# Kernel optimization log

Hardware: AMD Instinct MI355X
Metric: run time of the kernel (lower is better)

Reference implementation:

```python
import jax, jax.numpy as jnp
import numpy as np

N, E, G = 30000, 480000, 64
IN, H, L = 24, 512, 6


def setup_inputs() -> dict:
    key = jax.random.key(0)
    ks = jax.random.split(key, 20)
    s = 0.05
    inp = {
        "x": jax.random.normal(ks[0], (N, IN), dtype=jnp.float32),
        "edge_index": jax.random.randint(ks[1], (2, E), 0, N, dtype=jnp.int64),
        "batch": jnp.sort(jax.random.randint(ks[2], (N,), 0, G, dtype=jnp.int64)),
        # node encoder
        "enc_w": jax.random.normal(ks[3], (IN, H), dtype=jnp.float32) * s,
        "enc_b": jnp.zeros((H,), dtype=jnp.float32),
        # per-layer message MLP (stacked over L layers), weights stored [in, out]
        "mlp_w1": jax.random.normal(ks[4], (L, H, H), dtype=jnp.float32) * s,
        "mlp_b1": jnp.zeros((L, H), dtype=jnp.float32),
        "mlp_w2": jax.random.normal(ks[5], (L, H, H), dtype=jnp.float32) * s,
        "mlp_b2": jnp.zeros((L, H), dtype=jnp.float32),
        # per-layer GRUCell params, [in, 3H] layout (gates order: r, z, n)
        "gru_wih": jax.random.normal(ks[6], (L, H, 3 * H), dtype=jnp.float32) * s,
        "gru_whh": jax.random.normal(ks[7], (L, H, 3 * H), dtype=jnp.float32) * s,
        "gru_bih": jnp.zeros((L, 3 * H), dtype=jnp.float32),
        "gru_bhh": jnp.zeros((L, 3 * H), dtype=jnp.float32),
        # head MLP
        "head_w1": jax.random.normal(ks[8], (H, H // 2), dtype=jnp.float32) * s,
        "head_b1": jnp.zeros((H // 2,), dtype=jnp.float32),
        "head_w2": jax.random.normal(ks[9], (H // 2, 1), dtype=jnp.float32) * s,
        "head_b2": jnp.zeros((1,), dtype=jnp.float32),
    }
    return inp


def _forward(x, edge_index, batch, enc_w, enc_b, mlp_w1, mlp_b1, mlp_w2, mlp_b2,
             gru_wih, gru_whh, gru_bih, gru_bhh, head_w1, head_b1, head_w2, head_b2):
    src, dst = edge_index[0], edge_index[1]
    h = x @ enc_w + enc_b  # [N, H]
    for l in range(L):
        # message MLP depends only on x_j, so compute per-node then gather
        msg = jnp.maximum(h @ mlp_w1[l] + mlp_b1[l], 0.0) @ mlp_w2[l] + mlp_b2[l]  # [N, H]
        # scatter-add over edges + self-loop contribution (add_self_loops)
        m = jax.ops.segment_sum(msg[src], dst, num_segments=N) + msg  # [N, H]
        # GRUCell(input=m, hidden=h); torch gate order: reset, update, new
        gi = m @ gru_wih[l] + gru_bih[l]
        gh = h @ gru_whh[l] + gru_bhh[l]
        r = jax.nn.sigmoid(gi[:, :H] + gh[:, :H])
        z = jax.nn.sigmoid(gi[:, H:2 * H] + gh[:, H:2 * H])
        n = jnp.tanh(gi[:, 2 * H:] + r * gh[:, 2 * H:])
        h = (1.0 - z) * n + z * h
    # global mean pool per graph
    sums = jax.ops.segment_sum(h, batch, num_segments=G)
    cnt = jax.ops.segment_sum(jnp.ones((N,), dtype=h.dtype), batch, num_segments=G)
    pooled = sums / jnp.maximum(cnt, 1.0)[:, None]  # [G, H]
    out = jnp.maximum(pooled @ head_w1 + head_b1, 0.0) @ head_w2 + head_b2
    return out[:, 0]  # [G]


def reference(x, edge_index, batch, enc_w, enc_b, mlp_w1, mlp_b1, mlp_w2, mlp_b2,
              gru_wih, gru_whh, gru_bih, gru_bhh, head_w1, head_b1, head_w2, head_b2):
    return _forward(x, edge_index, batch, enc_w, enc_b, mlp_w1, mlp_b1, mlp_w2, mlp_b2,
                    gru_wih, gru_whh, gru_bih, gru_bhh, head_w1, head_b1, head_w2, head_b2)
```

## Files before the change

### kernel.cpp

```cpp
#include <hip/hip_runtime.h>
#include <hip/hip_bf16.h>
#include <math.h>

#define N_NODES 30000
#define N_EDGES 480000
#define N_GRAPH 64
#define DIN 24
#define HD 512
#define NL 6

typedef __hip_bfloat16 bf16;
using short8 = __attribute__((ext_vector_type(8))) short;
using f32x4 = __attribute__((ext_vector_type(4))) float;

#define ASYNC16(gp, lp)                                              \
    __builtin_amdgcn_global_load_lds(                                \
        (const __attribute__((address_space(1))) void*)(gp),         \
        (__attribute__((address_space(3))) void*)(lp), 16, 0, 0)

#define WAITALL_BAR()                                                \
    do {                                                             \
        asm volatile("s_waitcnt vmcnt(0) lgkmcnt(0)" ::: "memory");  \
        __builtin_amdgcn_sched_barrier(0);                           \
        __builtin_amdgcn_s_barrier();                                \
    } while (0)

__device__ __forceinline__ float sigmoidf_(float x) { return 1.0f / (1.0f + expf(-x)); }
__device__ __forceinline__ float b2f(unsigned short u) {
    return __uint_as_float(((unsigned int)u) << 16);
}
__device__ __forceinline__ unsigned short f2b(float f) {
    bf16 b = __float2bfloat16(f);
    return *(unsigned short*)&b;
}

__global__ __launch_bounds__(256) void enc_kernel(const float* __restrict__ x,
                                                  const float* __restrict__ w,
                                                  const float* __restrict__ b,
                                                  bf16* __restrict__ h) {
    __shared__ float xs[DIN];
    int row = blockIdx.x;
    int tid = threadIdx.x;
    if (tid < DIN) xs[tid] = x[row * DIN + tid];
    __syncthreads();
    for (int c = tid; c < HD; c += 256) {
        float acc = b[c];
#pragma unroll
        for (int k = 0; k < DIN; k++) acc = fmaf(xs[k], w[k * HD + c], acc);
        h[(size_t)row * HD + c] = __float2bfloat16(acc);
    }
}

__global__ __launch_bounds__(256) void twcvt_kernel(const float* __restrict__ W,
                                                    bf16* __restrict__ WtH,
                                                    bf16* __restrict__ WtL, int Nc) {
    __shared__ float s[32][33];
    int l = blockIdx.z;
    const float* Wp = W + (size_t)l * HD * Nc;
    size_t ob = (size_t)l * HD * Nc;
    int k0 = blockIdx.y * 32, c0 = blockIdx.x * 32;
    int tx = threadIdx.x & 31, ty = threadIdx.x >> 5;
    for (int r = ty; r < 32; r += 8) s[r][tx] = Wp[(size_t)(k0 + r) * Nc + c0 + tx];
    __syncthreads();
    for (int r = ty; r < 32; r += 8) {
        float v = s[tx][r];
        unsigned short hu = f2b(v);
        float hf = b2f(hu);
        size_t o = ob + (size_t)(c0 + r) * HD + k0 + tx;
        *(unsigned short*)&WtH[o] = hu;
        WtL[o] = __float2bfloat16(v - hf);
    }
}

template <bool RELU>
__global__ __launch_bounds__(256, 3) void gemm_mfma(const bf16* __restrict__ A,
                                                    const bf16* __restrict__ WtH,
                                                    const bf16* __restrict__ WtL,
                                                    const float* __restrict__ bias,
                                                    bf16* __restrict__ C, int n) {
    __shared__ __align__(16) bf16 SB[2][3 * 128 * 32];
    int tid = threadIdx.x;
    int wv = tid >> 6, lane = tid & 63;
    int quad = lane >> 4, l16 = lane & 15;
    int crow = lane >> 2, cseg = lane & 3;
    int gseg = cseg ^ ((crow >> 1) & 3);
    int fsw = (quad ^ ((l16 >> 1) & 3)) * 8;
    int row0 = blockIdx.y * 128, col0 = blockIdx.x * 128;
    f32x4 acc[2][8] = {};

    const bf16* gsrc[6];
#pragma unroll
    for (int j = 0; j < 6; j++) {
        int c = wv * 6 + j;
        if (c < 8) {
            int gr = row0 + c * 16 + crow;
            if (gr > n - 1) gr = n - 1;
            gsrc[j] = A + (size_t)gr * HD + gseg * 8;
        } else if (c < 16) {
            gsrc[j] = WtH + (size_t)(col0 + (c - 8) * 16 + crow) * HD + gseg * 8;
        } else {
            gsrc[j] = WtL + (size_t)(col0 + (c - 16) * 16 + crow) * HD + gseg * 8;
        }
    }
    auto stage = [&](int kt, int nb) {
#pragma unroll
        for (int j = 0; j < 6; j++) ASYNC16(gsrc[j] + kt, &SB[nb][(wv * 6 + j) * 512]);
    };

    stage(0, 0);
    for (int t16 = 0; t16 < 16; t16++) {
        int b = t16 & 1;
        WAITALL_BAR();
        if (t16 < 15) stage((t16 + 1) * 32, b ^ 1);
        short8 bfr[2][2];
#pragma unroll
        for (int t = 0; t < 2; t++) {
            int fo = ((wv * 2 + t) * 16 + l16) * 32 + fsw;
            bfr[t][0] = *(const short8*)&SB[b][4096 + fo];
            bfr[t][1] = *(const short8*)&SB[b][8192 + fo];
        }
        __builtin_amdgcn_s_setprio(1);
#pragma unroll
        for (int i = 0; i < 8; i++) {
            short8 af = *(const short8*)&SB[b][(i * 16 + l16) * 32 + fsw];
#pragma unroll
            for (int t = 0; t < 2; t++) {
                acc[t][i] = __builtin_amdgcn_mfma_f32_16x16x32_bf16(af, bfr[t][0], acc[t][i], 0, 0, 0);
                acc[t][i] = __builtin_amdgcn_mfma_f32_16x16x32_bf16(af, bfr[t][1], acc[t][i], 0, 0, 0);
            }
        }
        __builtin_amdgcn_s_setprio(0);
    }
    __syncthreads();
    bf16* Cs = (bf16*)SB;
#pragma unroll
    for (int t = 0; t < 2; t++) {
        int colL = (wv * 2 + t) * 16 + l16;
        float bb = bias[col0 + colL];
#pragma unroll
        for (int i = 0; i < 8; i++) {
#pragma unroll
            for (int r = 0; r < 4; r++) {
                int rowL = i * 16 + quad * 4 + r;
                float v = acc[t][i][r] + bb;
                if (RELU) v = fmaxf(v, 0.0f);
                Cs[rowL * 132 + colL] = __float2bfloat16(v);
            }
        }
    }
    __syncthreads();
    const unsigned short* cp = (const unsigned short*)Cs;
#pragma unroll
    for (int pass = 0; pass < 8; pass++) {
        int rowL = pass * 16 + (tid >> 4);
        int row = row0 + rowL;
        int cc = (tid & 15) * 8;
        if (row < n) {
            ushort4 a0 = *(const ushort4*)&cp[rowL * 132 + cc];
            ushort4 a1 = *(const ushort4*)&cp[rowL * 132 + cc + 4];
            uint4 ov;
            ov.x = ((unsigned int)a0.y << 16) | a0.x;
            ov.y = ((unsigned int)a0.w << 16) | a0.z;
            ov.z = ((unsigned int)a1.y << 16) | a1.x;
            ov.w = ((unsigned int)a1.w << 16) | a1.z;
            *(uint4*)&((unsigned short*)C)[(size_t)row * HD + col0 + cc] = ov;
        }
    }
}

__global__ __launch_bounds__(256, 2) void gru_mfma(const bf16* __restrict__ M,
                                                   const bf16* __restrict__ Hc,
                                                   const bf16* __restrict__ WiH,
                                                   const bf16* __restrict__ WiL,
                                                   const bf16* __restrict__ WhH,
                                                   const bf16* __restrict__ WhL,
                                                   const float* __restrict__ bih,
                                                   const float* __restrict__ bhh,
                                                   bf16* __restrict__ Hn, int n) {
    __shared__ __align__(16) bf16 Ms[128 * 32];
    __shared__ __align__(16) bf16 Hs[128 * 32];
    __shared__ __align__(16) bf16 Ws[12 * 64 * 32];
    int tid = threadIdx.x;
    int wv = tid >> 6, lane = tid & 63;
    int quad = lane >> 4, l16 = lane & 15;
    int crow = lane >> 2, cseg = lane & 3;
    int gseg = cseg ^ ((crow >> 1) & 3);
    int fsw = (quad ^ ((l16 >> 1) & 3)) * 8;
    int row0 = blockIdx.y * 128, col0 = blockIdx.x * 64;
    f32x4 aR[8] = {}, aZ[8] = {}, aI[8] = {}, aHn[8] = {};

    int moff[8];
    const bf16* wgp[4];
    int wlds[4];
    if (wv == 0) {
#pragma unroll
        for (int j = 0; j < 8; j++) {
            int gr = row0 + j * 16 + crow;
            if (gr > n - 1) gr = n - 1;
            moff[j] = gr * HD + gseg * 8;
        }
    } else {
        const bf16* wbase[4] = {WiH, WiL, WhH, WhL};
#pragma unroll
        for (int pp = 0; pp < 4; pp++) {
            int p = (wv - 1) * 4 + pp;
            int mat = (p >= 6);
            int q = p - mat * 6;
            int g = q >> 1, pl = q & 1;
            const bf16* base = wbase[mat * 2 + pl] + (size_t)(g * HD + col0) * HD;
            wgp[pp] = base + crow * HD + gseg * 8;
            wlds[pp] = p * 2048;
        }
    }

    int fo = (wv * 16 + l16) * 32 + fsw;
    for (int kt = 0; kt < 512; kt += 32) {
        if (wv == 0) {
#pragma unroll
            for (int j = 0; j < 8; j++) {
                ASYNC16(&M[moff[j] + kt], &Ms[j * 512]);
                ASYNC16(&Hc[moff[j] + kt], &Hs[j * 512]);
            }
        } else {
#pragma unroll
            for (int pp = 0; pp < 4; pp++)
#pragma unroll
                for (int s = 0; s < 4; s++)
                    ASYNC16(wgp[pp] + (size_t)s * 16 * HD + kt, &Ws[wlds[pp] + s * 512]);
        }
        __syncthreads();
        short8 wrh = *(const short8*)&Ws[0 * 2048 + fo];
        short8 wrl = *(const short8*)&Ws[1 * 2048 + fo];
        short8 wzh = *(const short8*)&Ws[2 * 2048 + fo];
        short8 wzl = *(const short8*)&Ws[3 * 2048 + fo];
        short8 wnh = *(const short8*)&Ws[4 * 2048 + fo];
        short8 wnl = *(const short8*)&Ws[5 * 2048 + fo];
        short8 vrh = *(const short8*)&Ws[6 * 2048 + fo];
        short8 vrl = *(const short8*)&Ws[7 * 2048 + fo];
        short8 vzh = *(const short8*)&Ws[8 * 2048 + fo];
        short8 vzl = *(const short8*)&Ws[9 * 2048 + fo];
        short8 vnh = *(const short8*)&Ws[10 * 2048 + fo];
        short8 vnl = *(const short8*)&Ws[11 * 2048 + fo];
#pragma unroll
        for (int i = 0; i < 8; i++) {
            short8 am = *(const short8*)&Ms[(i * 16 + l16) * 32 + fsw];
            short8 ah = *(const short8*)&Hs[(i * 16 + l16) * 32 + fsw];
            aR[i] = __builtin_amdgcn_mfma_f32_16x16x32_bf16(am, wrh, aR[i], 0, 0, 0);
            aR[i] = __builtin_amdgcn_mfma_f32_16x16x32_bf16(am, wrl, aR[i], 0, 0, 0);
            aR[i] = __builtin_amdgcn_mfma_f32_16x16x32_bf16(ah, vrh, aR[i], 0, 0, 0);
            aR[i] = __builtin_amdgcn_mfma_f32_16x16x32_bf16(ah, vrl, aR[i], 0, 0, 0);
            aZ[i] = __builtin_amdgcn_mfma_f32_16x16x32_bf16(am, wzh, aZ[i], 0, 0, 0);
            aZ[i] = __builtin_amdgcn_mfma_f32_16x16x32_bf16(am, wzl, aZ[i], 0, 0, 0);
            aZ[i] = __builtin_amdgcn_mfma_f32_16x16x32_bf16(ah, vzh, aZ[i], 0, 0, 0);
            aZ[i] = __builtin_amdgcn_mfma_f32_16x16x32_bf16(ah, vzl, aZ[i], 0, 0, 0);
            aI[i] = __builtin_amdgcn_mfma_f32_16x16x32_bf16(am, wnh, aI[i], 0, 0, 0);
            aI[i] = __builtin_amdgcn_mfma_f32_16x16x32_bf16(am, wnl, aI[i], 0, 0, 0);
            aHn[i] = __builtin_amdgcn_mfma_f32_16x16x32_bf16(ah, vnh, aHn[i], 0, 0, 0);
            aHn[i] = __builtin_amdgcn_mfma_f32_16x16x32_bf16(ah, vnl, aHn[i], 0, 0, 0);
        }
        __syncthreads();
    }
    float* Zs32 = (float*)Ws;
    float* Ps32 = Zs32 + 64 * 66;
    int colL = wv * 16 + l16;
    int col = col0 + colL;
    float brz = bih[col] + bhh[col];
    float bzz = bih[HD + col] + bhh[HD + col];
    float bin_ = bih[2 * HD + col];
    float bhn_ = bhh[2 * HD + col];
    const unsigned short* hp = (const unsigned short*)Hc;
    unsigned short* op = (unsigned short*)Hn;
#pragma unroll
    for (int hhalf = 0; hhalf < 2; hhalf++) {
#pragma unroll
        for (int i = 0; i < 4; i++) {
            int ii = hhalf * 4 + i;
#pragma unroll
            for (int r = 0; r < 4; r++) {
                int rowL = i * 16 + quad * 4 + r;
                float rg = sigmoidf_(aR[ii][r] + brz);
                float zg = sigmoidf_(aZ[ii][r] + bzz);
                float ng = tanhf(aI[ii][r] + bin_ + rg * (aHn[ii][r] + bhn_));
                Zs32[rowL * 66 + colL] = zg;
                Ps32[rowL * 66 + colL] = (1.0f - zg) * ng;
            }
        }
        __syncthreads();
#pragma unroll
        for (int sub = 0; sub < 2; sub++) {
            int rowL = sub * 32 + (tid >> 3);
            int row = row0 + hhalf * 64 + rowL;
            int cc = (tid & 7) * 8;
            if (row < n) {
                uint4 hv = *(const uint4*)&hp[(size_t)row * HD + col0 + cc];
                unsigned int hw[4] = {hv.x, hv.y, hv.z, hv.w};
                unsigned int ow[4];
#pragma unroll
                for (int q = 0; q < 4; q++) {
                    float h0 = b2f((unsigned short)(hw[q] & 0xffffu));
                    float h1 = b2f((unsigned short)(hw[q] >> 16));
                    float z0 = Zs32[rowL * 66 + cc + 2 * q];
                    float z1 = Zs32[rowL * 66 + cc + 2 * q + 1];
                    float p0 = Ps32[rowL * 66 + cc + 2 * q];
                    float p1 = Ps32[rowL * 66 + cc + 2 * q + 1];
                    float o0 = fmaf(z0, h0, p0);
                    float o1 = fmaf(z1, h1, p1);
                    ow[q] = ((unsigned int)f2b(o1) << 16) | f2b(o0);
                }
                uint4 ov = {ow[0], ow[1], ow[2], ow[3]};
                *(uint4*)&op[(size_t)row * HD + col0 + cc] = ov;
            }
        }
        __syncthreads();
    }
}

__global__ __launch_bounds__(256) void deg_kernel(const int* __restrict__ dst,
                                                  int* __restrict__ deg) {
    int e = blockIdx.x * 256 + threadIdx.x;
    if (e < N_EDGES) atomicAdd(&deg[dst[e]], 1);
}

__global__ __launch_bounds__(1024) void scan_kernel(const int* __restrict__ deg,
                                                    int* __restrict__ offs) {
    __shared__ int buf[1024];
    __shared__ int carry_s;
    int tid = threadIdx.x;
    if (tid == 0) carry_s = 0;
    __syncthreads();
    for (int base = 0; base < N_NODES; base += 1024) {
        int v = (base + tid < N_NODES) ? deg[base + tid] : 0;
        buf[tid] = v;
        __syncthreads();
        for (int s = 1; s < 1024; s <<= 1) {
            int t = (tid >= s) ? buf[tid - s] : 0;
            __syncthreads();
            buf[tid] += t;
            __syncthreads();
        }
        int incl = buf[tid];
        if (base + tid < N_NODES) offs[base + tid] = carry_s + incl - v;
        __syncthreads();
        if (tid == 0) carry_s += buf[1023];
        __syncthreads();
    }
    if (tid == 0) offs[N_NODES] = carry_s;
}

__global__ __launch_bounds__(256) void bucket_kernel(const int* __restrict__ src,
                                                     const int* __restrict__ dst,
                                                     const int* __restrict__ offs,
                                                     int* __restrict__ cursor,
                                                     unsigned short* __restrict__ elist) {
    int e = blockIdx.x * 256 + threadIdx.x;
    if (e >= N_EDGES) return;
    int d = dst[e];
    int pos = atomicAdd(&cursor[d], 1);
    elist[offs[d] + pos] = (unsigned short)src[e];
}

__global__ __launch_bounds__(256) void gather_kernel(const bf16* __restrict__ msg,
                                                     bf16* __restrict__ m,
                                                     const unsigned short* __restrict__ elist,
                                                     const int* __restrict__ offs) {
    int nid = blockIdx.x, tid = threadIdx.x;
    int beg = offs[nid], end = offs[nid + 1];
    const unsigned int* mp = (const unsigned int*)msg;
    unsigned int u = mp[(size_t)nid * 256 + tid];
    float ax = b2f((unsigned short)(u & 0xffffu));
    float ay = b2f((unsigned short)(u >> 16));
    int e = beg;
    for (; e + 3 < end; e += 4) {
        unsigned int v0 = mp[(size_t)elist[e] * 256 + tid];
        unsigned int v1 = mp[(size_t)elist[e + 1] * 256 + tid];
        unsigned int v2 = mp[(size_t)elist[e + 2] * 256 + tid];
        unsigned int v3 = mp[(size_t)elist[e + 3] * 256 + tid];
        ax += b2f((unsigned short)(v0 & 0xffffu)) + b2f((unsigned short)(v1 & 0xffffu)) +
              b2f((unsigned short)(v2 & 0xffffu)) + b2f((unsigned short)(v3 & 0xffffu));
        ay += b2f((unsigned short)(v0 >> 16)) + b2f((unsigned short)(v1 >> 16)) +
              b2f((unsigned short)(v2 >> 16)) + b2f((unsigned short)(v3 >> 16));
    }
    for (; e < end; e++) {
        unsigned int v0 = mp[(size_t)elist[e] * 256 + tid];
        ax += b2f((unsigned short)(v0 & 0xffffu));
        ay += b2f((unsigned short)(v0 >> 16));
    }
    unsigned int out = ((unsigned int)f2b(ay) << 16) | (unsigned int)f2b(ax);
    ((unsigned int*)m)[(size_t)nid * 256 + tid] = out;
}

__global__ __launch_bounds__(256) void pool_kernel(const bf16* __restrict__ h,
                                                   const int* __restrict__ batch,
                                                   float* __restrict__ pooled,
                                                   float* __restrict__ cnt) {
    int g = blockIdx.x;
    int col = blockIdx.y * 256 + threadIdx.x;
    int lo = 0, hi = N_NODES;
    while (lo < hi) { int mid = (lo + hi) >> 1; if (batch[mid] < g) lo = mid + 1; else hi = mid; }
    int gs = lo;
    hi = N_NODES;
    while (lo < hi) { int mid = (lo + hi) >> 1; if (batch[mid] < g + 1) lo = mid + 1; else hi = mid; }
    int ge = lo;
    const unsigned short* hp = (const unsigned short*)h;
    float acc = 0.0f;
    int r = gs;
    for (; r + 3 < ge; r += 4) {
        acc += b2f(hp[(size_t)r * HD + col]) + b2f(hp[(size_t)(r + 1) * HD + col]) +
               b2f(hp[(size_t)(r + 2) * HD + col]) + b2f(hp[(size_t)(r + 3) * HD + col]);
    }
    for (; r < ge; r++) acc += b2f(hp[(size_t)r * HD + col]);
    pooled[g * HD + col] = acc;
    if (blockIdx.y == 0 && threadIdx.x == 0) cnt[g] = (float)(ge - gs);
}

__global__ __launch_bounds__(256) void head_kernel(const float* __restrict__ pooled,
                                                   const float* __restrict__ cnt,
                                                   const float* __restrict__ w1,
                                                   const float* __restrict__ b1,
                                                   const float* __restrict__ w2,
                                                   const float* __restrict__ b2,
                                                   float* __restrict__ out) {
    __shared__ float prow[HD];
    __shared__ float red[256];
    int g = blockIdx.x, tid = threadIdx.x;
    float c = fmaxf(cnt[g], 1.0f);
    for (int j = tid; j < HD; j += 256) prow[j] = pooled[g * HD + j] / c;
    __syncthreads();
    float acc = b1[tid];
    for (int k = 0; k < HD; k++) acc = fmaf(prow[k], w1[k * 256 + tid], acc);
    red[tid] = fmaxf(acc, 0.0f) * w2[tid];
    __syncthreads();
    for (int s = 128; s > 0; s >>= 1) {
        if (tid < s) red[tid] += red[tid + s];
        __syncthreads();
    }
    if (tid == 0) out[g] = red[0] + b2[0];
}

extern "C" void kernel_launch(void* const* d_in, const int* in_sizes, int n_in,
                              void* d_out, int out_size, void* d_ws, size_t ws_size,
                              hipStream_t stream) {
    const float* x = (const float*)d_in[0];
    const int* eidx = (const int*)d_in[1];
    const int* batch = (const int*)d_in[2];
    const float* enc_w = (const float*)d_in[3];
    const float* enc_b = (const float*)d_in[4];
    const float* mlp_w1 = (const float*)d_in[5];
    const float* mlp_b1 = (const float*)d_in[6];
    const float* mlp_w2 = (const float*)d_in[7];
    const float* mlp_b2 = (const float*)d_in[8];
    const float* gru_wih = (const float*)d_in[9];
    const float* gru_whh = (const float*)d_in[10];
    const float* gru_bih = (const float*)d_in[11];
    const float* gru_bhh = (const float*)d_in[12];
    const float* head_w1 = (const float*)d_in[13];
    const float* head_b1 = (const float*)d_in[14];
    const float* head_w2 = (const float*)d_in[15];
    const float* head_b2 = (const float*)d_in[16];
    const int* src = eidx;
    const int* dst = eidx + N_EDGES;

    const size_t NH = (size_t)N_NODES * HD;
    char* p = (char*)d_ws;
    auto alloc = [&](size_t bytes) { char* q = p; p += (bytes + 255) & ~(size_t)255; return q; };
    bf16* S0 = (bf16*)alloc(NH * 2);
    bf16* S1 = (bf16*)alloc(NH * 2);
    bf16* S2 = (bf16*)alloc(NH * 2);
    bf16* w1tH = (bf16*)alloc((size_t)NL * HD * HD * 2);
    bf16* w1tL = (bf16*)alloc((size_t)NL * HD * HD * 2);
    bf16* w2tH = (bf16*)alloc((size_t)NL * HD * HD * 2);
    bf16* w2tL = (bf16*)alloc((size_t)NL * HD * HD * 2);
    bf16* wihtH = (bf16*)alloc((size_t)NL * 3 * HD * HD * 2);
    bf16* wihtL = (bf16*)alloc((size_t)NL * 3 * HD * HD * 2);
    bf16* whhtH = (bf16*)alloc((size_t)NL * 3 * HD * HD * 2);
    bf16* whhtL = (bf16*)alloc((size_t)NL * 3 * HD * HD * 2);
    float* pooled = (float*)alloc((size_t)N_GRAPH * HD * 4);
    float* cnt = (float*)alloc(N_GRAPH * 4);
    int* deg = (int*)alloc((N_NODES + 1) * 4);
    int* offs = (int*)alloc((N_NODES + 1) * 4);
    unsigned short* elist = (unsigned short*)alloc((size_t)N_EDGES * 2);

    twcvt_kernel<<<dim3(16, 16, NL), 256, 0, stream>>>(mlp_w1, w1tH, w1tL, HD);
    twcvt_kernel<<<dim3(16, 16, NL), 256, 0, stream>>>(mlp_w2, w2tH, w2tL, HD);
    twcvt_kernel<<<dim3(48, 16, NL), 256, 0, stream>>>(gru_wih, wihtH, wihtL, 3 * HD);
    twcvt_kernel<<<dim3(48, 16, NL), 256, 0, stream>>>(gru_whh, whhtH, whhtL, 3 * HD);

    hipMemsetAsync(deg, 0, (N_NODES + 1) * sizeof(int), stream);
    deg_kernel<<<(N_EDGES + 255) / 256, 256, 0, stream>>>(dst, deg);
    scan_kernel<<<1, 1024, 0, stream>>>(deg, offs);
    hipMemsetAsync(deg, 0, (N_NODES + 1) * sizeof(int), stream);
    bucket_kernel<<<(N_EDGES + 255) / 256, 256, 0, stream>>>(src, dst, offs, deg, elist);

    enc_kernel<<<N_NODES, 256, 0, stream>>>(x, enc_w, enc_b, S0);

    bf16* hcur = S0;
    bf16* hoth = S1;
    dim3 ggrid(4, (N_NODES + 127) / 128);
    dim3 ugrid(8, (N_NODES + 127) / 128);

    for (int l = 0; l < NL; l++) {
        size_t wsq = (size_t)l * HD * HD;
        size_t wgq = (size_t)l * 3 * HD * HD;
        const float* b1 = mlp_b1 + (size_t)l * HD;
        const float* b2 = mlp_b2 + (size_t)l * HD;
        const float* bih = gru_bih + (size_t)l * 3 * HD;
        const float* bhh = gru_bhh + (size_t)l * 3 * HD;

        gemm_mfma<true><<<ggrid, 256, 0, stream>>>(hcur, w1tH + wsq, w1tL + wsq, b1, hoth, N_NODES);
        gemm_mfma<false><<<ggrid, 256, 0, stream>>>(hoth, w2tH + wsq, w2tL + wsq, b2, S2, N_NODES);
        gather_kernel<<<N_NODES, 256, 0, stream>>>(S2, hoth, elist, offs);
        gru_mfma<<<ugrid, 256, 0, stream>>>(hoth, hcur, wihtH + wgq, wihtL + wgq,
                                            whhtH + wgq, whhtL + wgq, bih, bhh, S2, N_NODES);
        bf16* newh = S2;
        S2 = hcur;
        hcur = newh;
    }

    pool_kernel<<<dim3(N_GRAPH, 2), 256, 0, stream>>>(hcur, batch, pooled, cnt);
    head_kernel<<<N_GRAPH, 256, 0, stream>>>(pooled, cnt, head_w1, head_b1, head_w2, head_b2,
                                             (float*)d_out);
}
```

Measured before the change: 2.525 ms.

## Double row tile to 256 with 8-wave blocks in MLP and GRU GEMMs

Both MFMA kernels now use 512-thread blocks covering 256 rows instead of 128. The eight waves are arranged 2x4, so the same weight tiles in LDS serve twice as many rows, which halves weight traffic per row. Load duties are redistributed across the waves, and the epilogues are split into halves or quarters that reuse the smaller LDS scratch. The costs are a larger LDS footprint, more barriers in the epilogue, and fewer blocks overall, which may lower occupancy and give a worse tail over the 118-block grid.

```diff
diff --git a/kernel.cpp b/kernel.cpp
--- a/kernel.cpp
+++ b/kernel.cpp
@@ -73,38 +73,43 @@
 }
 
 template <bool RELU>
-__global__ __launch_bounds__(256, 3) void gemm_mfma(const bf16* __restrict__ A,
+__global__ __launch_bounds__(512, 2) void gemm_mfma(const bf16* __restrict__ A,
                                                     const bf16* __restrict__ WtH,
                                                     const bf16* __restrict__ WtL,
                                                     const float* __restrict__ bias,
                                                     bf16* __restrict__ C, int n) {
-    __shared__ __align__(16) bf16 SB[2][3 * 128 * 32];
+    __shared__ __align__(16) bf16 SB[2][16384];
     int tid = threadIdx.x;
     int wv = tid >> 6, lane = tid & 63;
+    int wr = wv >> 2, wc = wv & 3;
     int quad = lane >> 4, l16 = lane & 15;
     int crow = lane >> 2, cseg = lane & 3;
     int gseg = cseg ^ ((crow >> 1) & 3);
     int fsw = (quad ^ ((l16 >> 1) & 3)) * 8;
-    int row0 = blockIdx.y * 128, col0 = blockIdx.x * 128;
+    int row0 = blockIdx.y * 256, col0 = blockIdx.x * 128;
     f32x4 acc[2][8] = {};
 
-    const bf16* gsrc[6];
-#pragma unroll
-    for (int j = 0; j < 6; j++) {
-        int c = wv * 6 + j;
-        if (c < 8) {
+    const bf16* gsrc[4];
+    int glds[4];
+#pragma unroll
+    for (int j = 0; j < 4; j++) {
+        int c = wv * 4 + j;
+        if (c < 16) {
             int gr = row0 + c * 16 + crow;
             if (gr > n - 1) gr = n - 1;
             gsrc[j] = A + (size_t)gr * HD + gseg * 8;
-        } else if (c < 16) {
-            gsrc[j] = WtH + (size_t)(col0 + (c - 8) * 16 + crow) * HD + gseg * 8;
+            glds[j] = c * 512;
+        } else if (c < 24) {
+            gsrc[j] = WtH + (size_t)(col0 + (c - 16) * 16 + crow) * HD + gseg * 8;
+            glds[j] = 8192 + (c - 16) * 512;
         } else {
-            gsrc[j] = WtL + (size_t)(col0 + (c - 16) * 16 + crow) * HD + gseg * 8;
+            gsrc[j] = WtL + (size_t)(col0 + (c - 24) * 16 + crow) * HD + gseg * 8;
+            glds[j] = 12288 + (c - 24) * 512;
         }
     }
     auto stage = [&](int kt, int nb) {
 #pragma unroll
-        for (int j = 0; j < 6; j++) ASYNC16(gsrc[j] + kt, &SB[nb][(wv * 6 + j) * 512]);
+        for (int j = 0; j < 4; j++) ASYNC16(gsrc[j] + kt, &SB[nb][glds[j]]);
     };
 
     stage(0, 0);
@@ -115,14 +120,14 @@
         short8 bfr[2][2];
 #pragma unroll
         for (int t = 0; t < 2; t++) {
-            int fo = ((wv * 2 + t) * 16 + l16) * 32 + fsw;
-            bfr[t][0] = *(const short8*)&SB[b][4096 + fo];
-            bfr[t][1] = *(const short8*)&SB[b][8192 + fo];
+            int fo = ((wc * 2 + t) * 16 + l16) * 32 + fsw;
+            bfr[t][0] = *(const short8*)&SB[b][8192 + fo];
+            bfr[t][1] = *(const short8*)&SB[b][12288 + fo];
         }
         __builtin_amdgcn_s_setprio(1);
 #pragma unroll
         for (int i = 0; i < 8; i++) {
-            short8 af = *(const short8*)&SB[b][(i * 16 + l16) * 32 + fsw];
+            short8 af = *(const short8*)&SB[b][((wr * 8 + i) * 16 + l16) * 32 + fsw];
 #pragma unroll
             for (int t = 0; t < 2; t++) {
                 acc[t][i] = __builtin_amdgcn_mfma_f32_16x16x32_bf16(af, bfr[t][0], acc[t][i], 0, 0, 0);
@@ -133,42 +138,48 @@
     }
     __syncthreads();
     bf16* Cs = (bf16*)SB;
-#pragma unroll
-    for (int t = 0; t < 2; t++) {
-        int colL = (wv * 2 + t) * 16 + l16;
-        float bb = bias[col0 + colL];
-#pragma unroll
-        for (int i = 0; i < 8; i++) {
-#pragma unroll
-            for (int r = 0; r < 4; r++) {
-                int rowL = i * 16 + quad * 4 + r;
-                float v = acc[t][i][r] + bb;
-                if (RELU) v = fmaxf(v, 0.0f);
-                Cs[rowL * 132 + colL] = __float2bfloat16(v);
+    const unsigned short* cp = (const unsigned short*)Cs;
+#pragma unroll
+    for (int h = 0; h < 2; h++) {
+        if (wr == h) {
+#pragma unroll
+            for (int t = 0; t < 2; t++) {
+                int colL = (wc * 2 + t) * 16 + l16;
+                float bb = bias[col0 + colL];
+#pragma unroll
+                for (int i = 0; i < 8; i++) {
+#pragma unroll
+                    for (int r = 0; r < 4; r++) {
+                        int rowL = i * 16 + quad * 4 + r;
+                        float v = acc[t][i][r] + bb;
+                        if (RELU) v = fmaxf(v, 0.0f);
+                        Cs[rowL * 132 + colL] = __float2bfloat16(v);
+                    }
+                }
             }
         }
-    }
-    __syncthreads();
-    const unsigned short* cp = (const unsigned short*)Cs;
-#pragma unroll
-    for (int pass = 0; pass < 8; pass++) {
-        int rowL = pass * 16 + (tid >> 4);
-        int row = row0 + rowL;
-        int cc = (tid & 15) * 8;
-        if (row < n) {
-            ushort4 a0 = *(const ushort4*)&cp[rowL * 132 + cc];
-            ushort4 a1 = *(const ushort4*)&cp[rowL * 132 + cc + 4];
-            uint4 ov;
-            ov.x = ((unsigned int)a0.y << 16) | a0.x;
-            ov.y = ((unsigned int)a0.w << 16) | a0.z;
-            ov.z = ((unsigned int)a1.y << 16) | a1.x;
-            ov.w = ((unsigned int)a1.w << 16) | a1.z;
-            *(uint4*)&((unsigned short*)C)[(size_t)row * HD + col0 + cc] = ov;
-        }
-    }
-}
-
-__global__ __launch_bounds__(256, 2) void gru_mfma(const bf16* __restrict__ M,
+        __syncthreads();
+#pragma unroll
+        for (int pass = 0; pass < 4; pass++) {
+            int rowL = pass * 32 + (tid >> 4);
+            int row = row0 + h * 128 + rowL;
+            int cc = (tid & 15) * 8;
+            if (row < n) {
+                ushort4 a0 = *(const ushort4*)&cp[rowL * 132 + cc];
+                ushort4 a1 = *(const ushort4*)&cp[rowL * 132 + cc + 4];
+                uint4 ov;
+                ov.x = ((unsigned int)a0.y << 16) | a0.x;
+                ov.y = ((unsigned int)a0.w << 16) | a0.z;
+                ov.z = ((unsigned int)a1.y << 16) | a1.x;
+                ov.w = ((unsigned int)a1.w << 16) | a1.z;
+                *(uint4*)&((unsigned short*)C)[(size_t)row * HD + col0 + cc] = ov;
+            }
+        }
+        __syncthreads();
+    }
+}
+
+__global__ __launch_bounds__(512, 2) void gru_mfma(const bf16* __restrict__ M,
                                                    const bf16* __restrict__ Hc,
                                                    const bf16* __restrict__ WiH,
                                                    const bf16* __restrict__ WiL,
@@ -177,56 +188,58 @@
                                                    const float* __restrict__ bih,
                                                    const float* __restrict__ bhh,
                                                    bf16* __restrict__ Hn, int n) {
-    __shared__ __align__(16) bf16 Ms[128 * 32];
-    __shared__ __align__(16) bf16 Hs[128 * 32];
+    __shared__ __align__(16) bf16 Ms[256 * 32];
+    __shared__ __align__(16) bf16 Hs[256 * 32];
     __shared__ __align__(16) bf16 Ws[12 * 64 * 32];
     int tid = threadIdx.x;
     int wv = tid >> 6, lane = tid & 63;
+    int wr = wv >> 2, wc = wv & 3;
     int quad = lane >> 4, l16 = lane & 15;
     int crow = lane >> 2, cseg = lane & 3;
     int gseg = cseg ^ ((crow >> 1) & 3);
     int fsw = (quad ^ ((l16 >> 1) & 3)) * 8;
-    int row0 = blockIdx.y * 128, col0 = blockIdx.x * 64;
+    int row0 = blockIdx.y * 256, col0 = blockIdx.x * 64;
     f32x4 aR[8] = {}, aZ[8] = {}, aI[8] = {}, aHn[8] = {};
 
-    int moff[8];
-    const bf16* wgp[4];
-    int wlds[4];
-    if (wv == 0) {
+    const bf16* mhsrc[8];
+    bf16* mhdst[8];
+    const bf16* wgp[3];
+    int wldsb[3];
+    if (wv < 4) {
+        int mat = wv >> 1, half = wv & 1;
 #pragma unroll
         for (int j = 0; j < 8; j++) {
-            int gr = row0 + j * 16 + crow;
+            int ch = half * 8 + j;
+            int gr = row0 + ch * 16 + crow;
             if (gr > n - 1) gr = n - 1;
-            moff[j] = gr * HD + gseg * 8;
+            mhsrc[j] = (mat ? Hc : M) + (size_t)gr * HD + gseg * 8;
+            mhdst[j] = (mat ? Hs : Ms) + ch * 512;
         }
     } else {
         const bf16* wbase[4] = {WiH, WiL, WhH, WhL};
 #pragma unroll
-        for (int pp = 0; pp < 4; pp++) {
-            int p = (wv - 1) * 4 + pp;
+        for (int pp = 0; pp < 3; pp++) {
+            int p = (wv - 4) * 3 + pp;
             int mat = (p >= 6);
             int q = p - mat * 6;
             int g = q >> 1, pl = q & 1;
             const bf16* base = wbase[mat * 2 + pl] + (size_t)(g * HD + col0) * HD;
             wgp[pp] = base + crow * HD + gseg * 8;
-            wlds[pp] = p * 2048;
-        }
-    }
-
-    int fo = (wv * 16 + l16) * 32 + fsw;
+            wldsb[pp] = p * 2048;
+        }
+    }
+
+    int fo = (wc * 16 + l16) * 32 + fsw;
     for (int kt = 0; kt < 512; kt += 32) {
-        if (wv == 0) {
-#pragma unroll
-            for (int j = 0; j < 8; j++) {
-                ASYNC16(&M[moff[j] + kt], &Ms[j * 512]);
-                ASYNC16(&Hc[moff[j] + kt], &Hs[j * 512]);
-            }
+        if (wv < 4) {
+#pragma unroll
+            for (int j = 0; j < 8; j++) ASYNC16(mhsrc[j] + kt, mhdst[j]);
         } else {
 #pragma unroll
-            for (int pp = 0; pp < 4; pp++)
+            for (int pp = 0; pp < 3; pp++)
 #pragma unroll
                 for (int s = 0; s < 4; s++)
-                    ASYNC16(wgp[pp] + (size_t)s * 16 * HD + kt, &Ws[wlds[pp] + s * 512]);
+                    ASYNC16(wgp[pp] + (size_t)s * 16 * HD + kt, &Ws[wldsb[pp] + s * 512]);
         }
         __syncthreads();
         short8 wrh = *(const short8*)&Ws[0 * 2048 + fo];
@@ -243,8 +256,8 @@
         short8 vnl = *(const short8*)&Ws[11 * 2048 + fo];
 #pragma unroll
         for (int i = 0; i < 8; i++) {
-            short8 am = *(const short8*)&Ms[(i * 16 + l16) * 32 + fsw];
-            short8 ah = *(const short8*)&Hs[(i * 16 + l16) * 32 + fsw];
+            short8 am = *(const short8*)&Ms[((wr * 8 + i) * 16 + l16) * 32 + fsw];
+            short8 ah = *(const short8*)&Hs[((wr * 8 + i) * 16 + l16) * 32 + fsw];
             aR[i] = __builtin_amdgcn_mfma_f32_16x16x32_bf16(am, wrh, aR[i], 0, 0, 0);
             aR[i] = __builtin_amdgcn_mfma_f32_16x16x32_bf16(am, wrl, aR[i], 0, 0, 0);
             aR[i] = __builtin_amdgcn_mfma_f32_16x16x32_bf16(ah, vrh, aR[i], 0, 0, 0);
@@ -262,7 +275,7 @@
     }
     float* Zs32 = (float*)Ws;
     float* Ps32 = Zs32 + 64 * 66;
-    int colL = wv * 16 + l16;
+    int colL = wc * 16 + l16;
     int col = col0 + colL;
     float brz = bih[col] + bhh[col];
     float bzz = bih[HD + col] + bhh[HD + col];
@@ -271,25 +284,27 @@
     const unsigned short* hp = (const unsigned short*)Hc;
     unsigned short* op = (unsigned short*)Hn;
 #pragma unroll
-    for (int hhalf = 0; hhalf < 2; hhalf++) {
-#pragma unroll
-        for (int i = 0; i < 4; i++) {
-            int ii = hhalf * 4 + i;
-#pragma unroll
-            for (int r = 0; r < 4; r++) {
-                int rowL = i * 16 + quad * 4 + r;
-                float rg = sigmoidf_(aR[ii][r] + brz);
-                float zg = sigmoidf_(aZ[ii][r] + bzz);
-                float ng = tanhf(aI[ii][r] + bin_ + rg * (aHn[ii][r] + bhn_));
-                Zs32[rowL * 66 + colL] = zg;
-                Ps32[rowL * 66 + colL] = (1.0f - zg) * ng;
+    for (int h = 0; h < 4; h++) {
+        if (wr == (h >> 1)) {
+            int ib = (h & 1) * 4;
+#pragma unroll
+            for (int i2 = 0; i2 < 4; i2++) {
+                int i = ib + i2;
+#pragma unroll
+                for (int r = 0; r < 4; r++) {
+                    int rowL = i2 * 16 + quad * 4 + r;
+                    float rg = sigmoidf_(aR[i][r] + brz);
+                    float zg = sigmoidf_(aZ[i][r] + bzz);
+                    float ng = tanhf(aI[i][r] + bin_ + rg * (aHn[i][r] + bhn_));
+                    Zs32[rowL * 66 + colL] = zg;
+                    Ps32[rowL * 66 + colL] = (1.0f - zg) * ng;
+                }
             }
         }
         __syncthreads();
-#pragma unroll
-        for (int sub = 0; sub < 2; sub++) {
-            int rowL = sub * 32 + (tid >> 3);
-            int row = row0 + hhalf * 64 + rowL;
+        {
+            int rowL = tid >> 3;
+            int row = row0 + h * 64 + rowL;
             int cc = (tid & 7) * 8;
             if (row < n) {
                 uint4 hv = *(const uint4*)&hp[(size_t)row * HD + col0 + cc];
@@ -495,8 +510,8 @@
 
     bf16* hcur = S0;
     bf16* hoth = S1;
-    dim3 ggrid(4, (N_NODES + 127) / 128);
-    dim3 ugrid(8, (N_NODES + 127) / 128);
+    dim3 ggrid(4, (N_NODES + 255) / 256);
+    dim3 ugrid(8, (N_NODES + 255) / 256);
 
     for (int l = 0; l < NL; l++) {
         size_t wsq = (size_t)l * HD * HD;
@@ -506,10 +521,10 @@
         const float* bih = gru_bih + (size_t)l * 3 * HD;
         const float* bhh = gru_bhh + (size_t)l * 3 * HD;
 
-        gemm_mfma<true><<<ggrid, 256, 0, stream>>>(hcur, w1tH + wsq, w1tL + wsq, b1, hoth, N_NODES);
-        gemm_mfma<false><<<ggrid, 256, 0, stream>>>(hoth, w2tH + wsq, w2tL + wsq, b2, S2, N_NODES);
+        gemm_mfma<true><<<ggrid, 512, 0, stream>>>(hcur, w1tH + wsq, w1tL + wsq, b1, hoth, N_NODES);
+        gemm_mfma<false><<<ggrid, 512, 0, stream>>>(hoth, w2tH + wsq, w2tL + wsq, b2, S2, N_NODES);
         gather_kernel<<<N_NODES, 256, 0, stream>>>(S2, hoth, elist, offs);
-        gru_mfma<<<ugrid, 256, 0, stream>>>(hoth, hcur, wihtH + wgq, wihtL + wgq,
+        gru_mfma<<<ugrid, 512, 0, stream>>>(hoth, hcur, wihtH + wgq, wihtL + wgq,
                                             whhtH + wgq, whhtL + wgq, bih, bhh, S2, N_NODES);
         bf16* newh = S2;
         S2 = hcur;
```

Result: slower. 3.037 ms (+20.3%).

## Remap GEMM/GRU blocks by XCD and load 64-wide activation K-tiles

Applied to the files above, without the earlier changes.

Replaces the 2D grids with a 1D grid whose block IDs are remapped so blocks sharing a row band land on the same XCD, to improve L2 reuse of activation rows. Activation tiles are now staged 64 K-columns at a time with a new XOR swizzle, loaded every other iteration. The double-buffered pipeline in gemm_mfma is dropped for single-buffer load-then-sync steps, and occupancy bounds rise to 4. It also raises MFMA priority in the GRU loop. Losing the prefetch overlap may expose memory latency, and there is leftover dead code.

```diff
diff --git a/kernel.cpp b/kernel.cpp
--- a/kernel.cpp
+++ b/kernel.cpp
@@ -8,6 +8,7 @@
 #define DIN 24
 #define HD 512
 #define NL 6
+#define NRG 235
 
 typedef __hip_bfloat16 bf16;
 using short8 = __attribute__((ext_vector_type(8))) short;
@@ -17,13 +18,6 @@
     __builtin_amdgcn_global_load_lds(                                \
         (const __attribute__((address_space(1))) void*)(gp),         \
         (__attribute__((address_space(3))) void*)(lp), 16, 0, 0)
-
-#define WAITALL_BAR()                                                \
-    do {                                                             \
-        asm volatile("s_waitcnt vmcnt(0) lgkmcnt(0)" ::: "memory");  \
-        __builtin_amdgcn_sched_barrier(0);                           \
-        __builtin_amdgcn_s_barrier();                                \
-    } while (0)
 
 __device__ __forceinline__ float sigmoidf_(float x) { return 1.0f / (1.0f + expf(-x)); }
 __device__ __forceinline__ float b2f(unsigned short u) {
@@ -73,56 +67,81 @@
 }
 
 template <bool RELU>
-__global__ __launch_bounds__(256, 3) void gemm_mfma(const bf16* __restrict__ A,
+__global__ __launch_bounds__(256, 4) void gemm_mfma(const bf16* __restrict__ A,
                                                     const bf16* __restrict__ WtH,
                                                     const bf16* __restrict__ WtL,
                                                     const float* __restrict__ bias,
                                                     bf16* __restrict__ C, int n) {
-    __shared__ __align__(16) bf16 SB[2][3 * 128 * 32];
+    __shared__ __align__(16) bf16 GS[16896];
+    int id = blockIdx.x;
+    int xcd = id & 7, kb = id >> 3;
+    int bx = kb & 3;
+    int by = (kb >> 2) * 8 + xcd;
+    if (by >= (n + 127) / 128) return;
+    int row0 = by * 128, col0 = bx * 128;
+
     int tid = threadIdx.x;
     int wv = tid >> 6, lane = tid & 63;
     int quad = lane >> 4, l16 = lane & 15;
     int crow = lane >> 2, cseg = lane & 3;
     int gseg = cseg ^ ((crow >> 1) & 3);
     int fsw = (quad ^ ((l16 >> 1) & 3)) * 8;
-    int row0 = blockIdx.y * 128, col0 = blockIdx.x * 128;
+    int r7 = lane >> 3, s3 = lane & 7;
+    int keyr = ((r7 & 1) << 2) | ((r7 >> 1) & 3);
+    int sseg = s3 ^ keyr;
+    int mkey = ((l16 & 1) << 2) | ((l16 >> 1) & 3);
     f32x4 acc[2][8] = {};
 
-    const bf16* gsrc[6];
-#pragma unroll
-    for (int j = 0; j < 6; j++) {
-        int c = wv * 6 + j;
-        if (c < 8) {
-            int gr = row0 + c * 16 + crow;
+    int gro[8];
+    if (wv < 2) {
+#pragma unroll
+        for (int j = 0; j < 8; j++) {
+            int c = wv * 8 + j;
+            int gr = row0 + c * 8 + r7;
             if (gr > n - 1) gr = n - 1;
-            gsrc[j] = A + (size_t)gr * HD + gseg * 8;
-        } else if (c < 16) {
-            gsrc[j] = WtH + (size_t)(col0 + (c - 8) * 16 + crow) * HD + gseg * 8;
+            gro[j] = gr * HD + sseg * 8;
+        }
+    } else {
+        const bf16* wb = (wv == 2) ? WtH : WtL;
+#pragma unroll
+        for (int j = 0; j < 8; j++)
+            gro[j] = 0;
+#pragma unroll
+        for (int s = 0; s < 8; s++) { }
+    }
+    int boff[8];
+    const bf16* wb = (wv == 2) ? WtH : WtL;
+    if (wv >= 2) {
+#pragma unroll
+        for (int s = 0; s < 8; s++) boff[s] = (col0 + s * 16 + crow) * HD + gseg * 8;
+    }
+    bf16* bdst = GS + ((wv == 2) ? 8192 : 12288);
+
+    for (int kt = 0; kt < 512; kt += 32) {
+        int kk = (kt >> 5) & 1;
+        if (wv < 2) {
+            if (kk == 0) {
+#pragma unroll
+                for (int j = 0; j < 8; j++)
+                    ASYNC16(&A[gro[j] + kt], &GS[(wv * 8 + j) * 512]);
+            }
         } else {
-            gsrc[j] = WtL + (size_t)(col0 + (c - 16) * 16 + crow) * HD + gseg * 8;
-        }
-    }
-    auto stage = [&](int kt, int nb) {
-#pragma unroll
-        for (int j = 0; j < 6; j++) ASYNC16(gsrc[j] + kt, &SB[nb][(wv * 6 + j) * 512]);
-    };
-
-    stage(0, 0);
-    for (int t16 = 0; t16 < 16; t16++) {
-        int b = t16 & 1;
-        WAITALL_BAR();
-        if (t16 < 15) stage((t16 + 1) * 32, b ^ 1);
+#pragma unroll
+            for (int s = 0; s < 8; s++) ASYNC16(&wb[boff[s] + kt], &bdst[s * 512]);
+        }
+        __syncthreads();
         short8 bfr[2][2];
 #pragma unroll
         for (int t = 0; t < 2; t++) {
             int fo = ((wv * 2 + t) * 16 + l16) * 32 + fsw;
-            bfr[t][0] = *(const short8*)&SB[b][4096 + fo];
-            bfr[t][1] = *(const short8*)&SB[b][8192 + fo];
-        }
+            bfr[t][0] = *(const short8*)&GS[8192 + fo];
+            bfr[t][1] = *(const short8*)&GS[12288 + fo];
+        }
+        int aoffk = (((kk << 2) + quad) ^ mkey) * 8;
         __builtin_amdgcn_s_setprio(1);
 #pragma unroll
         for (int i = 0; i < 8; i++) {
-            short8 af = *(const short8*)&SB[b][(i * 16 + l16) * 32 + fsw];
+            short8 af = *(const short8*)&GS[(i * 16 + l16) * 64 + aoffk];
 #pragma unroll
             for (int t = 0; t < 2; t++) {
                 acc[t][i] = __builtin_amdgcn_mfma_f32_16x16x32_bf16(af, bfr[t][0], acc[t][i], 0, 0, 0);
@@ -130,9 +149,9 @@
             }
         }
         __builtin_amdgcn_s_setprio(0);
-    }
-    __syncthreads();
-    bf16* Cs = (bf16*)SB;
+        __syncthreads();
+    }
+    bf16* Cs = GS;
 #pragma unroll
     for (int t = 0; t < 2; t++) {
         int colL = (wv * 2 + t) * 16 + l16;
@@ -177,27 +196,38 @@
                                                    const float* __restrict__ bih,
                                                    const float* __restrict__ bhh,
                                                    bf16* __restrict__ Hn, int n) {
-    __shared__ __align__(16) bf16 Ms[128 * 32];
-    __shared__ __align__(16) bf16 Hs[128 * 32];
+    __shared__ __align__(16) bf16 Ms[128 * 64];
+    __shared__ __align__(16) bf16 Hs[128 * 64];
     __shared__ __align__(16) bf16 Ws[12 * 64 * 32];
+    int id = blockIdx.x;
+    int xcd = id & 7, kb = id >> 3;
+    int band = xcd >> 1, colg = xcd & 1;
+    int bx = colg * 4 + (kb & 3);
+    int by = (kb >> 2) * 4 + band;
+    if (by >= (n + 127) / 128) return;
+    int row0 = by * 128, col0 = bx * 64;
+
     int tid = threadIdx.x;
     int wv = tid >> 6, lane = tid & 63;
     int quad = lane >> 4, l16 = lane & 15;
     int crow = lane >> 2, cseg = lane & 3;
     int gseg = cseg ^ ((crow >> 1) & 3);
     int fsw = (quad ^ ((l16 >> 1) & 3)) * 8;
-    int row0 = blockIdx.y * 128, col0 = blockIdx.x * 64;
+    int r7 = lane >> 3, s3 = lane & 7;
+    int keyr = ((r7 & 1) << 2) | ((r7 >> 1) & 3);
+    int sseg = s3 ^ keyr;
+    int mkey = ((l16 & 1) << 2) | ((l16 >> 1) & 3);
     f32x4 aR[8] = {}, aZ[8] = {}, aI[8] = {}, aHn[8] = {};
 
-    int moff[8];
+    int gro[16];
     const bf16* wgp[4];
     int wlds[4];
     if (wv == 0) {
 #pragma unroll
-        for (int j = 0; j < 8; j++) {
-            int gr = row0 + j * 16 + crow;
+        for (int c = 0; c < 16; c++) {
+            int gr = row0 + c * 8 + r7;
             if (gr > n - 1) gr = n - 1;
-            moff[j] = gr * HD + gseg * 8;
+            gro[c] = gr * HD + sseg * 8;
         }
     } else {
         const bf16* wbase[4] = {WiH, WiL, WhH, WhL};
@@ -215,11 +245,14 @@
 
     int fo = (wv * 16 + l16) * 32 + fsw;
     for (int kt = 0; kt < 512; kt += 32) {
+        int kk = (kt >> 5) & 1;
         if (wv == 0) {
-#pragma unroll
-            for (int j = 0; j < 8; j++) {
-                ASYNC16(&M[moff[j] + kt], &Ms[j * 512]);
-                ASYNC16(&Hc[moff[j] + kt], &Hs[j * 512]);
+            if (kk == 0) {
+#pragma unroll
+                for (int c = 0; c < 16; c++) {
+                    ASYNC16(&M[gro[c] + kt], &Ms[c * 512]);
+                    ASYNC16(&Hc[gro[c] + kt], &Hs[c * 512]);
+                }
             }
         } else {
 #pragma unroll
@@ -241,10 +274,12 @@
         short8 vzl = *(const short8*)&Ws[9 * 2048 + fo];
         short8 vnh = *(const short8*)&Ws[10 * 2048 + fo];
         short8 vnl = *(const short8*)&Ws[11 * 2048 + fo];
+        int aoffk = (((kk << 2) + quad) ^ mkey) * 8;
+        __builtin_amdgcn_s_setprio(1);
 #pragma unroll
         for (int i = 0; i < 8; i++) {
-            short8 am = *(const short8*)&Ms[(i * 16 + l16) * 32 + fsw];
-            short8 ah = *(const short8*)&Hs[(i * 16 + l16) * 32 + fsw];
+            short8 am = *(const short8*)&Ms[(i * 16 + l16) * 64 + aoffk];
+            short8 ah = *(const short8*)&Hs[(i * 16 + l16) * 64 + aoffk];
             aR[i] = __builtin_amdgcn_mfma_f32_16x16x32_bf16(am, wrh, aR[i], 0, 0, 0);
             aR[i] = __builtin_amdgcn_mfma_f32_16x16x32_bf16(am, wrl, aR[i], 0, 0, 0);
             aR[i] = __builtin_amdgcn_mfma_f32_16x16x32_bf16(ah, vrh, aR[i], 0, 0, 0);
@@ -258,6 +293,7 @@
             aHn[i] = __builtin_amdgcn_mfma_f32_16x16x32_bf16(ah, vnh, aHn[i], 0, 0, 0);
             aHn[i] = __builtin_amdgcn_mfma_f32_16x16x32_bf16(ah, vnl, aHn[i], 0, 0, 0);
         }
+        __builtin_amdgcn_s_setprio(0);
         __syncthreads();
     }
     float* Zs32 = (float*)Ws;
@@ -495,8 +531,8 @@
 
     bf16* hcur = S0;
     bf16* hoth = S1;
-    dim3 ggrid(4, (N_NODES + 127) / 128);
-    dim3 ugrid(8, (N_NODES + 127) / 128);
+    int ggrid = 8 * ((NRG + 7) / 8) * 4;
+    int ugrid = 8 * ((NRG + 3) / 4) * 4;
 
     for (int l = 0; l < NL; l++) {
         size_t wsq = (size_t)l * HD * HD;
```

Result: faster. 2.406 ms (-4.7%).

## Deepen async LDS prefetch pipelines and remap blocks to XCDs in GEMM and GRU

Applied to the files above, without the earlier changes.

The MLP GEMM now prefetches two k-tiles ahead and waits on a partial vmcnt rather than draining all loads at every step. The GRU kernel gains double-buffered M/H tiles, spreads loading across all waves, and issues the next weight tile after its fragments are read into registers. Both kernels switch to a 1D grid with XCD-aware block-to-tile mapping so blocks sharing A rows land on the same XCD's L2. This adds barriers per iteration and some idle blocks from the rounded grid.

```diff
diff --git a/kernel.cpp b/kernel.cpp
--- a/kernel.cpp
+++ b/kernel.cpp
@@ -8,6 +8,7 @@
 #define DIN 24
 #define HD 512
 #define NL 6
+#define NRG 235
 
 typedef __hip_bfloat16 bf16;
 using short8 = __attribute__((ext_vector_type(8))) short;
@@ -18,12 +19,7 @@
         (const __attribute__((address_space(1))) void*)(gp),         \
         (__attribute__((address_space(3))) void*)(lp), 16, 0, 0)
 
-#define WAITALL_BAR()                                                \
-    do {                                                             \
-        asm volatile("s_waitcnt vmcnt(0) lgkmcnt(0)" ::: "memory");  \
-        __builtin_amdgcn_sched_barrier(0);                           \
-        __builtin_amdgcn_s_barrier();                                \
-    } while (0)
+#define SCHED_FENCE() __builtin_amdgcn_sched_barrier(0)
 
 __device__ __forceinline__ float sigmoidf_(float x) { return 1.0f / (1.0f + expf(-x)); }
 __device__ __forceinline__ float b2f(unsigned short u) {
@@ -78,17 +74,24 @@
                                                     const bf16* __restrict__ WtL,
                                                     const float* __restrict__ bias,
                                                     bf16* __restrict__ C, int n) {
-    __shared__ __align__(16) bf16 SB[2][3 * 128 * 32];
+    __shared__ __align__(16) bf16 SB[2][12288];
+    int id = blockIdx.x;
+    int xcd = id & 7, kb = id >> 3;
+    int bx = kb & 3;
+    int by = (kb >> 2) * 8 + xcd;
+    if (by >= (n + 127) / 128) return;
+    int row0 = by * 128, col0 = bx * 128;
+
     int tid = threadIdx.x;
     int wv = tid >> 6, lane = tid & 63;
     int quad = lane >> 4, l16 = lane & 15;
     int crow = lane >> 2, cseg = lane & 3;
     int gseg = cseg ^ ((crow >> 1) & 3);
     int fsw = (quad ^ ((l16 >> 1) & 3)) * 8;
-    int row0 = blockIdx.y * 128, col0 = blockIdx.x * 128;
     f32x4 acc[2][8] = {};
 
     const bf16* gsrc[6];
+    int glds[6];
 #pragma unroll
     for (int j = 0; j < 6; j++) {
         int c = wv * 6 + j;
@@ -96,22 +99,29 @@
             int gr = row0 + c * 16 + crow;
             if (gr > n - 1) gr = n - 1;
             gsrc[j] = A + (size_t)gr * HD + gseg * 8;
+            glds[j] = c * 512;
         } else if (c < 16) {
             gsrc[j] = WtH + (size_t)(col0 + (c - 8) * 16 + crow) * HD + gseg * 8;
+            glds[j] = 4096 + (c - 8) * 512;
         } else {
             gsrc[j] = WtL + (size_t)(col0 + (c - 16) * 16 + crow) * HD + gseg * 8;
+            glds[j] = 8192 + (c - 16) * 512;
         }
     }
     auto stage = [&](int kt, int nb) {
 #pragma unroll
-        for (int j = 0; j < 6; j++) ASYNC16(gsrc[j] + kt, &SB[nb][(wv * 6 + j) * 512]);
+        for (int j = 0; j < 6; j++) ASYNC16(gsrc[j] + kt, &SB[nb][glds[j]]);
     };
 
     stage(0, 0);
+    stage(32, 1);
     for (int t16 = 0; t16 < 16; t16++) {
         int b = t16 & 1;
-        WAITALL_BAR();
-        if (t16 < 15) stage((t16 + 1) * 32, b ^ 1);
+        if (t16 == 15) asm volatile("s_waitcnt vmcnt(0)" ::: "memory");
+        else           asm volatile("s_waitcnt vmcnt(6)" ::: "memory");
+        SCHED_FENCE();
+        __builtin_amdgcn_s_barrier();
+        SCHED_FENCE();
         short8 bfr[2][2];
 #pragma unroll
         for (int t = 0; t < 2; t++) {
@@ -130,8 +140,12 @@
             }
         }
         __builtin_amdgcn_s_setprio(0);
-    }
-    __syncthreads();
+        asm volatile("s_waitcnt lgkmcnt(0)" ::: "memory");
+        SCHED_FENCE();
+        __builtin_amdgcn_s_barrier();
+        SCHED_FENCE();
+        if (t16 < 14) stage((t16 + 2) * 32, b);
+    }
     bf16* Cs = (bf16*)SB;
 #pragma unroll
     for (int t = 0; t < 2; t++) {
@@ -177,58 +191,76 @@
                                                    const float* __restrict__ bih,
                                                    const float* __restrict__ bhh,
                                                    bf16* __restrict__ Hn, int n) {
-    __shared__ __align__(16) bf16 Ms[128 * 32];
-    __shared__ __align__(16) bf16 Hs[128 * 32];
+    __shared__ __align__(16) bf16 Ms[2][128 * 32];
+    __shared__ __align__(16) bf16 Hs[2][128 * 32];
     __shared__ __align__(16) bf16 Ws[12 * 64 * 32];
+    int id = blockIdx.x;
+    int xcd = id & 7, kb = id >> 3;
+    int band = xcd >> 1, colg = xcd & 1;
+    int bx = colg * 4 + (kb & 3);
+    int by = (kb >> 2) * 4 + band;
+    if (by >= (n + 127) / 128) return;
+    int row0 = by * 128, col0 = bx * 64;
+
     int tid = threadIdx.x;
     int wv = tid >> 6, lane = tid & 63;
     int quad = lane >> 4, l16 = lane & 15;
     int crow = lane >> 2, cseg = lane & 3;
     int gseg = cseg ^ ((crow >> 1) & 3);
     int fsw = (quad ^ ((l16 >> 1) & 3)) * 8;
-    int row0 = blockIdx.y * 128, col0 = blockIdx.x * 64;
     f32x4 aR[8] = {}, aZ[8] = {}, aI[8] = {}, aHn[8] = {};
 
-    int moff[8];
-    const bf16* wgp[4];
-    int wlds[4];
-    if (wv == 0) {
-#pragma unroll
-        for (int j = 0; j < 8; j++) {
-            int gr = row0 + j * 16 + crow;
-            if (gr > n - 1) gr = n - 1;
-            moff[j] = gr * HD + gseg * 8;
-        }
-    } else {
-        const bf16* wbase[4] = {WiH, WiL, WhH, WhL};
-#pragma unroll
-        for (int pp = 0; pp < 4; pp++) {
-            int p = (wv - 1) * 4 + pp;
-            int mat = (p >= 6);
-            int q = p - mat * 6;
-            int g = q >> 1, pl = q & 1;
-            const bf16* base = wbase[mat * 2 + pl] + (size_t)(g * HD + col0) * HD;
-            wgp[pp] = base + crow * HD + gseg * 8;
-            wlds[pp] = p * 2048;
-        }
-    }
-
+    const bf16* mhsrc[4];
+    int mhrch[4];
+    int mhmat[4];
+#pragma unroll
+    for (int j = 0; j < 4; j++) {
+        int c = wv * 4 + j;
+        int mat = c >> 3, rch = c & 7;
+        int gr = row0 + rch * 16 + crow;
+        if (gr > n - 1) gr = n - 1;
+        mhsrc[j] = (mat ? Hc : M) + (size_t)gr * HD + gseg * 8;
+        mhrch[j] = rch * 512;
+        mhmat[j] = mat;
+    }
+    const bf16* wbase[4] = {WiH, WiL, WhH, WhL};
+    const bf16* wgp[3];
+    int wldsb[3];
+#pragma unroll
+    for (int pp = 0; pp < 3; pp++) {
+        int p = wv * 3 + pp;
+        int mat = (p >= 6);
+        int q = p - mat * 6;
+        int g = q >> 1, pl = q & 1;
+        const bf16* base = wbase[mat * 2 + pl] + (size_t)(g * HD + col0) * HD;
+        wgp[pp] = base + crow * HD + gseg * 8;
+        wldsb[pp] = p * 2048;
+    }
+    auto stageMH = [&](int kt, int nb) {
+#pragma unroll
+        for (int j = 0; j < 4; j++)
+            ASYNC16(mhsrc[j] + kt, (mhmat[j] ? &Hs[nb][mhrch[j]] : &Ms[nb][mhrch[j]]));
+    };
+    auto stageW = [&](int kt) {
+#pragma unroll
+        for (int pp = 0; pp < 3; pp++)
+#pragma unroll
+            for (int s = 0; s < 4; s++)
+                ASYNC16(wgp[pp] + (size_t)s * 16 * HD + kt, &Ws[wldsb[pp] + s * 512]);
+    };
+
+    stageMH(0, 0);
+    stageW(0);
+    stageMH(32, 1);
     int fo = (wv * 16 + l16) * 32 + fsw;
-    for (int kt = 0; kt < 512; kt += 32) {
-        if (wv == 0) {
-#pragma unroll
-            for (int j = 0; j < 8; j++) {
-                ASYNC16(&M[moff[j] + kt], &Ms[j * 512]);
-                ASYNC16(&Hc[moff[j] + kt], &Hs[j * 512]);
-            }
-        } else {
-#pragma unroll
-            for (int pp = 0; pp < 4; pp++)
-#pragma unroll
-                for (int s = 0; s < 4; s++)
-                    ASYNC16(wgp[pp] + (size_t)s * 16 * HD + kt, &Ws[wlds[pp] + s * 512]);
-        }
-        __syncthreads();
+    for (int t16 = 0; t16 < 16; t16++) {
+        int b = t16 & 1;
+        int kt = t16 * 32;
+        if (t16 == 15) asm volatile("s_waitcnt vmcnt(0)" ::: "memory");
+        else           asm volatile("s_waitcnt vmcnt(4)" ::: "memory");
+        SCHED_FENCE();
+        __builtin_amdgcn_s_barrier();
+        SCHED_FENCE();
         short8 wrh = *(const short8*)&Ws[0 * 2048 + fo];
         short8 wrl = *(const short8*)&Ws[1 * 2048 + fo];
         short8 wzh = *(const short8*)&Ws[2 * 2048 + fo];
@@ -241,10 +273,16 @@
         short8 vzl = *(const short8*)&Ws[9 * 2048 + fo];
         short8 vnh = *(const short8*)&Ws[10 * 2048 + fo];
         short8 vnl = *(const short8*)&Ws[11 * 2048 + fo];
+        asm volatile("s_waitcnt lgkmcnt(0)" ::: "memory");
+        SCHED_FENCE();
+        __builtin_amdgcn_s_barrier();
+        SCHED_FENCE();
+        if (t16 < 15) stageW(kt + 32);
+        __builtin_amdgcn_s_setprio(1);
 #pragma unroll
         for (int i = 0; i < 8; i++) {
-            short8 am = *(const short8*)&Ms[(i * 16 + l16) * 32 + fsw];
-            short8 ah = *(const short8*)&Hs[(i * 16 + l16) * 32 + fsw];
+            short8 am = *(const short8*)&Ms[b][(i * 16 + l16) * 32 + fsw];
+            short8 ah = *(const short8*)&Hs[b][(i * 16 + l16) * 32 + fsw];
             aR[i] = __builtin_amdgcn_mfma_f32_16x16x32_bf16(am, wrh, aR[i], 0, 0, 0);
             aR[i] = __builtin_amdgcn_mfma_f32_16x16x32_bf16(am, wrl, aR[i], 0, 0, 0);
             aR[i] = __builtin_amdgcn_mfma_f32_16x16x32_bf16(ah, vrh, aR[i], 0, 0, 0);
@@ -258,7 +296,12 @@
             aHn[i] = __builtin_amdgcn_mfma_f32_16x16x32_bf16(ah, vnh, aHn[i], 0, 0, 0);
             aHn[i] = __builtin_amdgcn_mfma_f32_16x16x32_bf16(ah, vnl, aHn[i], 0, 0, 0);
         }
-        __syncthreads();
+        __builtin_amdgcn_s_setprio(0);
+        asm volatile("s_waitcnt lgkmcnt(0)" ::: "memory");
+        SCHED_FENCE();
+        __builtin_amdgcn_s_barrier();
+        SCHED_FENCE();
+        if (t16 < 14) stageMH(kt + 64, b);
     }
     float* Zs32 = (float*)Ws;
     float* Ps32 = Zs32 + 64 * 66;
@@ -495,8 +538,8 @@
 
     bf16* hcur = S0;
     bf16* hoth = S1;
-    dim3 ggrid(4, (N_NODES + 127) / 128);
-    dim3 ugrid(8, (N_NODES + 127) / 128);
+    int ggrid = 8 * ((NRG + 7) / 8) * 4;
+    int ugrid = 8 * ((NRG + 3) / 4) * 4;
 
     for (int l = 0; l < NL; l++) {
         size_t wsq = (size_t)l * HD * HD;
```

After: 2.431 ms. 3.7% less time.
